# Performance work log

Hardware: AMD Instinct MI355X
Metric: run time of the kernel (lower is better)

The kernel has to match this reference:

```python
import jax, jax.numpy as jnp
import numpy as np


def setup_inputs() -> dict:
    key = jax.random.key(0)
    k1, k2 = jax.random.split(key)
    B, C, O, N = 16, 16, 16, 256
    in_tensor = jax.random.normal(k1, (B, C, N, N, 2), dtype=jnp.float32)
    # xavier_normal_ on (C, O, 15): fan_in = O*15, fan_out = C*15 (torch convention)
    std = (2.0 / (O * 15 + C * 15)) ** 0.5
    weights = jax.random.normal(k2, (C, O, 15), dtype=jnp.float32) * std
    return {"in_tensor": in_tensor, "weights": weights}


def reference(in_tensor, weights):
    # in_tensor: (B, C, N, N, 2); weights: (C, O, 15); default mode (real scalar per basis)
    B, C, N, _, _ = in_tensor.shape
    O = weights.shape[1]
    idx = jnp.arange(N)

    # diag: (B, C, N, 2); col/row sums: (B, C, N, 2)
    diag = jnp.swapaxes(jnp.diagonal(in_tensor, axis1=2, axis2=3), 2, 3)
    col_sum = in_tensor.sum(axis=2)
    row_sum = in_tensor.sum(axis=3)

    # class 3 maps: default mode uses only weight index 13 (index 14 unused, as in source)
    t = jnp.einsum('co,bcijk->boijk', weights[..., 13], in_tensor)
    out = t + jnp.swapaxes(t, 2, 3)

    def class1(out, v, A):
        # v: (B, C, 2), A: (C, O, 2)
        u0 = jnp.einsum('co,bck->bok', A[..., 0], v)  # broadcast everywhere
        u1 = jnp.einsum('co,bck->bok', A[..., 1], v)  # on diagonal
        out = out + u0[:, :, None, None, :]
        out = out.at[:, :, idx, idx, :].add(
            jnp.broadcast_to(u1[:, :, None, :], (B, O, N, 2)))
        return out

    def class2(out, v, A):
        # v: (B, C, N, 2), A: (C, O, 3)
        d = jnp.einsum('co,bcmk->bomk', A[..., 0], v)  # diagonal values
        r = jnp.einsum('co,bcmk->bomk', A[..., 1], v)  # broadcast over rows (index j)
        c = jnp.einsum('co,bcmk->bomk', A[..., 2], v)  # broadcast over cols (index i)
        out = out.at[:, :, idx, idx, :].add(d)
        out = out + r[:, :, None, :, :]
        out = out + c[:, :, :, None, :]
        return out

    out = class1(out, diag.mean(axis=2), weights[..., 0:2])
    out = class1(out, in_tensor.sum(axis=(2, 3)), weights[..., 0:2])
    out = class2(out, diag, weights[..., 4:7])
    out = class2(out, col_sum, weights[..., 7:10])
    out = class2(out, row_sum, weights[..., 10:13])
    return out
```

## Files before the change

kernel.cpp:

```cpp
#include <hip/hip_runtime.h>

#define NN 256
#define CC 16
#define OO 16
#define BB 16
#define NTILE 16
#define NPAIRS 136

#define OFF_DIAG 0
#define OFF_COL  131072
#define OFF_ROW  262144
#define OFF_TOT  393216
#define OFF_DSUM 393728
#define OFF_RI   394496
#define OFF_CJ   525568
#define OFF_DM   656640
#define OFF_S0   787712

__device__ __forceinline__ float2 nt_load2(const float2* p) {
    double d = __builtin_nontemporal_load((const double*)p);
    float2 r; *(double*)&r = d; return r;
}
__device__ __forceinline__ void nt_store2(float2* p, float2 v) {
    double d; *(float2*)&d = v;
    __builtin_nontemporal_store(d, (double*)p);
}

__global__ __launch_bounds__(1024) void k_reduce(const float* __restrict__ in,
                                                 float* __restrict__ ws) {
    float* diagA = ws + OFF_DIAG;
    float* colA  = ws + OFF_COL;
    float* rowA  = ws + OFF_ROW;
    float* totA  = ws + OFF_TOT;
    float* dsumA = ws + OFF_DSUM;

    const int bc  = blockIdx.x;
    const int tid = threadIdx.x;
    const int wv  = tid >> 6;
    const int ln  = tid & 63;

    const float* base = in + (size_t)bc * (NN * NN * 2);

    __shared__ float colLDS[16][512];
    __shared__ float rowLDS[512];
    __shared__ float diagLDS[512];
    __shared__ float redT[16][2];
    __shared__ float redD[16][2];

    float a0 = 0, a1 = 0, a2 = 0, a3 = 0;
    float b0 = 0, b1 = 0, b2 = 0, b3 = 0;
    float dsx = 0, dsy = 0;

    for (int i = wv; i < NN; i += 16) {
        const float4* rowp = (const float4*)(base + i * (NN * 2));
        float4 v0 = rowp[ln];
        float4 v1 = rowp[64 + ln];
        a0 += v0.x; a1 += v0.y; a2 += v0.z; a3 += v0.w;
        b0 += v1.x; b1 += v1.y; b2 += v1.z; b3 += v1.w;
        float sx = v0.x + v0.z + v1.x + v1.z;
        float sy = v0.y + v0.w + v1.y + v1.w;
#pragma unroll
        for (int off = 32; off >= 1; off >>= 1) {
            sx += __shfl_xor(sx, off);
            sy += __shfl_xor(sy, off);
        }
        if (ln == 0) { rowLDS[i * 2] = sx; rowLDS[i * 2 + 1] = sy; }
        int k4 = i >> 1;
        if (ln == (k4 & 63)) {
            float4 dv = (k4 >> 6) ? v1 : v0;
            float dx = (i & 1) ? dv.z : dv.x;
            float dy = (i & 1) ? dv.w : dv.y;
            diagLDS[i * 2] = dx; diagLDS[i * 2 + 1] = dy;
            dsx += dx; dsy += dy;
        }
    }
    colLDS[wv][4 * ln]       = a0; colLDS[wv][4 * ln + 1]       = a1;
    colLDS[wv][4 * ln + 2]   = a2; colLDS[wv][4 * ln + 3]       = a3;
    colLDS[wv][256 + 4 * ln]     = b0; colLDS[wv][256 + 4 * ln + 1] = b1;
    colLDS[wv][256 + 4 * ln + 2] = b2; colLDS[wv][256 + 4 * ln + 3] = b3;

#pragma unroll
    for (int off = 32; off >= 1; off >>= 1) {
        dsx += __shfl_xor(dsx, off);
        dsy += __shfl_xor(dsy, off);
    }
    if (ln == 0) { redD[wv][0] = dsx; redD[wv][1] = dsy; }
    __syncthreads();

    float totpart = 0.f;
    if (tid < 512) {
        float s = 0.f;
#pragma unroll
        for (int w2 = 0; w2 < 16; w2++) s += colLDS[w2][tid];
        colA[bc * 512 + tid]  = s;
        rowA[bc * 512 + tid]  = rowLDS[tid];
        diagA[bc * 512 + tid] = diagLDS[tid];
        totpart = s;
    }
#pragma unroll
    for (int off = 32; off >= 2; off >>= 1) totpart += __shfl_xor(totpart, off);
    if (ln < 2) redT[wv][ln] = totpart;
    __syncthreads();
    if (tid == 0) {
        float t0 = 0, t1 = 0, d0 = 0, d1 = 0;
        for (int w2 = 0; w2 < 16; w2++) {
            t0 += redT[w2][0]; t1 += redT[w2][1];
            d0 += redD[w2][0]; d1 += redD[w2][1];
        }
        totA[bc * 2]  = t0; totA[bc * 2 + 1]  = t1;
        dsumA[bc * 2] = d0; dsumA[bc * 2 + 1] = d1;
    }
}

__global__ __launch_bounds__(256) void k_terms(const float* __restrict__ w,
                                               float* __restrict__ ws) {
    const float* diagA = ws + OFF_DIAG;
    const float* colA  = ws + OFF_COL;
    const float* rowA  = ws + OFF_ROW;
    const float* totA  = ws + OFF_TOT;
    const float* dsumA = ws + OFF_DSUM;
    float* RiA = ws + OFF_RI;
    float* CjA = ws + OFF_CJ;
    float* DmA = ws + OFF_DM;
    float* S0A = ws + OFF_S0;

    const int b = blockIdx.x >> 4;
    const int o = blockIdx.x & 15;
    const int m = threadIdx.x;

    __shared__ float wL[CC][15];
    if (m < CC * 15) wL[m / 15][m % 15] = w[(m / 15) * (OO * 15) + o * 15 + m % 15];
    __syncthreads();

    float rix = 0, riy = 0, cjx = 0, cjy = 0, dmx = 0, dmy = 0;
    float s0x = 0, s0y = 0, dcx = 0, dcy = 0;
#pragma unroll
    for (int c = 0; c < CC; c++) {
        int bcm = (b * CC + c) * NN + m;
        float2 dg = ((const float2*)diagA)[bcm];
        float2 cs = ((const float2*)colA)[bcm];
        float2 rs = ((const float2*)rowA)[bcm];
        float w4 = wL[c][4], w5 = wL[c][5], w6 = wL[c][6];
        float w7 = wL[c][7], w8 = wL[c][8], w9 = wL[c][9];
        float wa = wL[c][10], wb = wL[c][11], wc = wL[c][12];
        rix += w6 * dg.x + w9 * cs.x + wc * rs.x;
        riy += w6 * dg.y + w9 * cs.y + wc * rs.y;
        cjx += w5 * dg.x + w8 * cs.x + wb * rs.x;
        cjy += w5 * dg.y + w8 * cs.y + wb * rs.y;
        dmx += w4 * dg.x + w7 * cs.x + wa * rs.x;
        dmy += w4 * dg.y + w7 * cs.y + wa * rs.y;
        float2 tt = ((const float2*)totA)[b * CC + c];
        float2 dd = ((const float2*)dsumA)[b * CC + c];
        float vx = dd.x * (1.0f / NN) + tt.x;
        float vy = dd.y * (1.0f / NN) + tt.y;
        s0x += wL[c][0] * vx; s0y += wL[c][0] * vy;
        dcx += wL[c][1] * vx; dcy += wL[c][1] * vy;
    }
    int om = (b * OO + o) * NN + m;
    ((float2*)RiA)[om] = make_float2(rix, riy);
    ((float2*)CjA)[om] = make_float2(cjx, cjy);
    ((float2*)DmA)[om] = make_float2(dmx + dcx, dmy + dcy);
    if (m == 0) ((float2*)S0A)[b * OO + o] = make_float2(s0x, s0y);
}

__global__ __launch_bounds__(256) void k_main(const float* __restrict__ in,
                                              const float* __restrict__ w,
                                              float* __restrict__ out,
                                              const float* __restrict__ ws) {
    const float* RiA  = ws + OFF_RI;
    const float* CjA  = ws + OFF_CJ;
    const float* DmA  = ws + OFF_DM;
    const float* S0A  = ws + OFF_S0;

    const int b = blockIdx.x / NPAIRS;
    int p = blockIdx.x % NPAIRS;
    int I = 0;
    { int cnt = NTILE; while (p >= cnt) { p -= cnt; cnt--; I++; } }
    const int J = I + p;

    const int tid = threadIdx.x;
    const int ti = tid >> 4;
    const int tj = tid & 15;

    __shared__ float  xch[256 * 34];
    __shared__ float  wsm[256];
    __shared__ float2 s0L[16];
    __shared__ float2 RiI[16][16];
    __shared__ float2 CjJ[16][16];
    __shared__ float2 RiJ[16][16];
    __shared__ float2 CjI[16][16];

    {
        wsm[tid] = w[tid * 15 + 13];
        RiI[ti][tj] = ((const float2*)RiA)[(b * OO + ti) * NN + I * 16 + tj];
        CjJ[ti][tj] = ((const float2*)CjA)[(b * OO + ti) * NN + J * 16 + tj];
        if (I != J) {
            RiJ[ti][tj] = ((const float2*)RiA)[(b * OO + ti) * NN + J * 16 + tj];
            CjI[ti][tj] = ((const float2*)CjA)[(b * OO + ti) * NN + I * 16 + tj];
        }
        if (tid < 16) s0L[tid] = ((const float2*)S0A)[b * OO + tid];
    }
    __syncthreads();

    float2 P[16], Q[16];
#pragma unroll
    for (int o = 0; o < 16; o++) { P[o] = make_float2(0.f, 0.f); Q[o] = make_float2(0.f, 0.f); }

    const float2* pA = (const float2*)in + ((b * CC) * NN + I * 16 + ti) * NN + J * 16 + tj;
    const float2* pB = (const float2*)in + ((b * CC) * NN + J * 16 + ti) * NN + I * 16 + tj;

#pragma unroll 8
    for (int c = 0; c < CC; c++) {
        float2 a  = nt_load2(&pA[c * (NN * NN)]);
        float2 bb = nt_load2(&pB[c * (NN * NN)]);
#pragma unroll
        for (int o = 0; o < 16; o++) {
            float wv = wsm[c * 16 + o];
            P[o].x += wv * a.x;  P[o].y += wv * a.y;
            Q[o].x += wv * bb.x; Q[o].y += wv * bb.y;
        }
    }

    const int sidx = ti * 16 + (tj ^ ti);
    const int ridx = tj * 16 + (ti ^ tj);
    const bool dgl = (I == J) && (ti == tj);

#pragma unroll
    for (int o = 0; o < 16; o++) *(float2*)&xch[sidx * 34 + o * 2] = Q[o];
    __syncthreads();
    {
        const int gi = I * 16 + ti, gj = J * 16 + tj;
#pragma unroll
        for (int o = 0; o < 16; o++) {
            float2 qt = *(const float2*)&xch[ridx * 34 + o * 2];
            float2 s0 = s0L[o];
            float2 ri = RiI[o][ti];
            float2 cj = CjJ[o][tj];
            float vx = P[o].x + qt.x + s0.x + ri.x + cj.x;
            float vy = P[o].y + qt.y + s0.y + ri.y + cj.y;
            if (dgl) {
                float2 dm = ((const float2*)DmA)[(b * OO + o) * NN + gi];
                vx += dm.x; vy += dm.y;
            }
            nt_store2(((float2*)out) + ((b * OO + o) * NN + gi) * NN + gj,
                      make_float2(vx, vy));
        }
    }

    if (I == J) return;

    __syncthreads();

#pragma unroll
    for (int o = 0; o < 16; o++) *(float2*)&xch[sidx * 34 + o * 2] = P[o];
    __syncthreads();
    {
        const int gi = J * 16 + ti, gj = I * 16 + tj;
#pragma unroll
        for (int o = 0; o < 16; o++) {
            float2 pt = *(const float2*)&xch[ridx * 34 + o * 2];
            float2 s0 = s0L[o];
            float2 ri = RiJ[o][ti];
            float2 cj = CjI[o][tj];
            float vx = Q[o].x + pt.x + s0.x + ri.x + cj.x;
            float vy = Q[o].y + pt.y + s0.y + ri.y + cj.y;
            nt_store2(((float2*)out) + ((b * OO + o) * NN + gi) * NN + gj,
                      make_float2(vx, vy));
        }
    }
}

extern "C" void kernel_launch(void* const* d_in, const int* in_sizes, int n_in,
                              void* d_out, int out_size, void* d_ws, size_t ws_size,
                              hipStream_t stream) {
    const float* in = (const float*)d_in[0];
    const float* w  = (const float*)d_in[1];
    float* out = (float*)d_out;
    float* ws  = (float*)d_ws;

    hipLaunchKernelGGL(k_reduce, dim3(BB * CC), dim3(1024), 0, stream, in, ws);
    hipLaunchKernelGGL(k_terms,  dim3(BB * OO), dim3(256),  0, stream, w, ws);
    hipLaunchKernelGGL(k_main,   dim3(BB * NPAIRS), dim3(256), 0, stream, in, w, out, ws);
}
```

Measured before the change: 266.3 us.

## Split reduce blocks in half, shrink main-kernel LDS exchange, fold S0 into Ri

The reduction kernel now splits each (b,c) plane into two half-plane blocks, which doubles the grid to 512 blocks for better CU coverage. Partial column sums and totals are written to separate buffers and combined in k_terms. The main kernel folds the S0 scalar into the Ri term. It also exchanges the transposed tile in two 8-channel chunks through a half-size LDS buffer, uses packed float2 vector arithmetic, and sets launch bounds for 4 blocks per CU to raise occupancy. The cost is extra barriers in the epilogue and extra partial-sum reads in k_terms.

```diff
diff --git a/kernel.cpp b/kernel.cpp
--- a/kernel.cpp
+++ b/kernel.cpp
@@ -7,43 +7,53 @@
 #define NTILE 16
 #define NPAIRS 136
 
-#define OFF_DIAG 0
-#define OFF_COL  131072
-#define OFF_ROW  262144
-#define OFF_TOT  393216
-#define OFF_DSUM 393728
-#define OFF_RI   394496
-#define OFF_CJ   525568
-#define OFF_DM   656640
-#define OFF_S0   787712
-
-__device__ __forceinline__ float2 nt_load2(const float2* p) {
+#define OFF_DIAG  0
+#define OFF_ROW   131072
+#define OFF_COL0  262144
+#define OFF_COL1  393216
+#define OFF_TOT0  524288
+#define OFF_TOT1  524800
+#define OFF_DSUM0 525312
+#define OFF_DSUM1 525824
+#define OFF_RI    526336
+#define OFF_CJ    657408
+#define OFF_DM    788480
+
+typedef float v2f __attribute__((ext_vector_type(2)));
+
+__device__ __forceinline__ v2f nt_loadv(const float2* p) {
     double d = __builtin_nontemporal_load((const double*)p);
-    float2 r; *(double*)&r = d; return r;
-}
-__device__ __forceinline__ void nt_store2(float2* p, float2 v) {
-    double d; *(float2*)&d = v;
+    v2f r; __builtin_memcpy(&r, &d, 8); return r;
+}
+__device__ __forceinline__ void nt_storev(float2* p, v2f v) {
+    double d; __builtin_memcpy(&d, &v, 8);
     __builtin_nontemporal_store(d, (double*)p);
+}
+__device__ __forceinline__ v2f ld2(const float* p) {
+    v2f r; __builtin_memcpy(&r, p, 8); return r;
 }
 
 __global__ __launch_bounds__(1024) void k_reduce(const float* __restrict__ in,
                                                  float* __restrict__ ws) {
     float* diagA = ws + OFF_DIAG;
-    float* colA  = ws + OFF_COL;
     float* rowA  = ws + OFF_ROW;
-    float* totA  = ws + OFF_TOT;
-    float* dsumA = ws + OFF_DSUM;
-
-    const int bc  = blockIdx.x;
+
+    const int bid  = blockIdx.x;
+    const int bc   = bid >> 1;
+    const int half = bid & 1;
+    float* colH  = ws + (half ? OFF_COL1 : OFF_COL0);
+    float* totH  = ws + (half ? OFF_TOT1 : OFF_TOT0);
+    float* dsumH = ws + (half ? OFF_DSUM1 : OFF_DSUM0);
+
     const int tid = threadIdx.x;
     const int wv  = tid >> 6;
     const int ln  = tid & 63;
 
-    const float* base = in + (size_t)bc * (NN * NN * 2);
+    const float* base = in + (size_t)bc * (NN * NN * 2) + (size_t)half * (128 * NN * 2);
 
     __shared__ float colLDS[16][512];
-    __shared__ float rowLDS[512];
-    __shared__ float diagLDS[512];
+    __shared__ float rowLDS[256];
+    __shared__ float diagLDS[256];
     __shared__ float redT[16][2];
     __shared__ float redD[16][2];
 
@@ -51,7 +61,10 @@
     float b0 = 0, b1 = 0, b2 = 0, b3 = 0;
     float dsx = 0, dsy = 0;
 
-    for (int i = wv; i < NN; i += 16) {
+#pragma unroll 2
+    for (int k = 0; k < 8; k++) {
+        const int i = wv + 16 * k;
+        const int g = (half << 7) + i;
         const float4* rowp = (const float4*)(base + i * (NN * 2));
         float4 v0 = rowp[ln];
         float4 v1 = rowp[64 + ln];
@@ -64,20 +77,18 @@
             sx += __shfl_xor(sx, off);
             sy += __shfl_xor(sy, off);
         }
-        if (ln == 0) { rowLDS[i * 2] = sx; rowLDS[i * 2 + 1] = sy; }
-        int k4 = i >> 1;
+        if (ln == 0) { rowLDS[2 * i] = sx; rowLDS[2 * i + 1] = sy; }
+        const int k4 = g >> 1;
         if (ln == (k4 & 63)) {
-            float4 dv = (k4 >> 6) ? v1 : v0;
-            float dx = (i & 1) ? dv.z : dv.x;
-            float dy = (i & 1) ? dv.w : dv.y;
-            diagLDS[i * 2] = dx; diagLDS[i * 2 + 1] = dy;
+            float4 dv = (k4 & 64) ? v1 : v0;
+            float dx = (g & 1) ? dv.z : dv.x;
+            float dy = (g & 1) ? dv.w : dv.y;
+            diagLDS[2 * i] = dx; diagLDS[2 * i + 1] = dy;
             dsx += dx; dsy += dy;
         }
     }
-    colLDS[wv][4 * ln]       = a0; colLDS[wv][4 * ln + 1]       = a1;
-    colLDS[wv][4 * ln + 2]   = a2; colLDS[wv][4 * ln + 3]       = a3;
-    colLDS[wv][256 + 4 * ln]     = b0; colLDS[wv][256 + 4 * ln + 1] = b1;
-    colLDS[wv][256 + 4 * ln + 2] = b2; colLDS[wv][256 + 4 * ln + 3] = b3;
+    ((float4*)&colLDS[wv][0])[ln]   = make_float4(a0, a1, a2, a3);
+    ((float4*)&colLDS[wv][256])[ln] = make_float4(b0, b1, b2, b3);
 
 #pragma unroll
     for (int off = 32; off >= 1; off >>= 1) {
@@ -92,10 +103,12 @@
         float s = 0.f;
 #pragma unroll
         for (int w2 = 0; w2 < 16; w2++) s += colLDS[w2][tid];
-        colA[bc * 512 + tid]  = s;
-        rowA[bc * 512 + tid]  = rowLDS[tid];
-        diagA[bc * 512 + tid] = diagLDS[tid];
+        colH[bc * 512 + tid] = s;
         totpart = s;
+    }
+    if (tid < 256) {
+        rowA[bc * 512 + half * 256 + tid]  = rowLDS[tid];
+        diagA[bc * 512 + half * 256 + tid] = diagLDS[tid];
     }
 #pragma unroll
     for (int off = 32; off >= 2; off >>= 1) totpart += __shfl_xor(totpart, off);
@@ -107,22 +120,24 @@
             t0 += redT[w2][0]; t1 += redT[w2][1];
             d0 += redD[w2][0]; d1 += redD[w2][1];
         }
-        totA[bc * 2]  = t0; totA[bc * 2 + 1]  = t1;
-        dsumA[bc * 2] = d0; dsumA[bc * 2 + 1] = d1;
+        totH[bc * 2]  = t0; totH[bc * 2 + 1]  = t1;
+        dsumH[bc * 2] = d0; dsumH[bc * 2 + 1] = d1;
     }
 }
 
 __global__ __launch_bounds__(256) void k_terms(const float* __restrict__ w,
                                                float* __restrict__ ws) {
     const float* diagA = ws + OFF_DIAG;
-    const float* colA  = ws + OFF_COL;
     const float* rowA  = ws + OFF_ROW;
-    const float* totA  = ws + OFF_TOT;
-    const float* dsumA = ws + OFF_DSUM;
+    const float* colA0 = ws + OFF_COL0;
+    const float* colA1 = ws + OFF_COL1;
+    const float* tot0  = ws + OFF_TOT0;
+    const float* tot1  = ws + OFF_TOT1;
+    const float* dsm0  = ws + OFF_DSUM0;
+    const float* dsm1  = ws + OFF_DSUM1;
     float* RiA = ws + OFF_RI;
     float* CjA = ws + OFF_CJ;
     float* DmA = ws + OFF_DM;
-    float* S0A = ws + OFF_S0;
 
     const int b = blockIdx.x >> 4;
     const int o = blockIdx.x & 15;
@@ -138,39 +153,41 @@
     for (int c = 0; c < CC; c++) {
         int bcm = (b * CC + c) * NN + m;
         float2 dg = ((const float2*)diagA)[bcm];
-        float2 cs = ((const float2*)colA)[bcm];
+        float2 c0 = ((const float2*)colA0)[bcm];
+        float2 c1 = ((const float2*)colA1)[bcm];
         float2 rs = ((const float2*)rowA)[bcm];
+        float csx = c0.x + c1.x, csy = c0.y + c1.y;
         float w4 = wL[c][4], w5 = wL[c][5], w6 = wL[c][6];
         float w7 = wL[c][7], w8 = wL[c][8], w9 = wL[c][9];
         float wa = wL[c][10], wb = wL[c][11], wc = wL[c][12];
-        rix += w6 * dg.x + w9 * cs.x + wc * rs.x;
-        riy += w6 * dg.y + w9 * cs.y + wc * rs.y;
-        cjx += w5 * dg.x + w8 * cs.x + wb * rs.x;
-        cjy += w5 * dg.y + w8 * cs.y + wb * rs.y;
-        dmx += w4 * dg.x + w7 * cs.x + wa * rs.x;
-        dmy += w4 * dg.y + w7 * cs.y + wa * rs.y;
-        float2 tt = ((const float2*)totA)[b * CC + c];
-        float2 dd = ((const float2*)dsumA)[b * CC + c];
-        float vx = dd.x * (1.0f / NN) + tt.x;
-        float vy = dd.y * (1.0f / NN) + tt.y;
+        rix += w6 * dg.x + w9 * csx + wc * rs.x;
+        riy += w6 * dg.y + w9 * csy + wc * rs.y;
+        cjx += w5 * dg.x + w8 * csx + wb * rs.x;
+        cjy += w5 * dg.y + w8 * csy + wb * rs.y;
+        dmx += w4 * dg.x + w7 * csx + wa * rs.x;
+        dmy += w4 * dg.y + w7 * csy + wa * rs.y;
+        float2 ta = ((const float2*)tot0)[b * CC + c];
+        float2 tb = ((const float2*)tot1)[b * CC + c];
+        float2 da = ((const float2*)dsm0)[b * CC + c];
+        float2 db = ((const float2*)dsm1)[b * CC + c];
+        float vx = (da.x + db.x) * (1.0f / NN) + ta.x + tb.x;
+        float vy = (da.y + db.y) * (1.0f / NN) + ta.y + tb.y;
         s0x += wL[c][0] * vx; s0y += wL[c][0] * vy;
         dcx += wL[c][1] * vx; dcy += wL[c][1] * vy;
     }
     int om = (b * OO + o) * NN + m;
-    ((float2*)RiA)[om] = make_float2(rix, riy);
+    ((float2*)RiA)[om] = make_float2(rix + s0x, riy + s0y);
     ((float2*)CjA)[om] = make_float2(cjx, cjy);
     ((float2*)DmA)[om] = make_float2(dmx + dcx, dmy + dcy);
-    if (m == 0) ((float2*)S0A)[b * OO + o] = make_float2(s0x, s0y);
-}
-
-__global__ __launch_bounds__(256) void k_main(const float* __restrict__ in,
-                                              const float* __restrict__ w,
-                                              float* __restrict__ out,
-                                              const float* __restrict__ ws) {
-    const float* RiA  = ws + OFF_RI;
-    const float* CjA  = ws + OFF_CJ;
-    const float* DmA  = ws + OFF_DM;
-    const float* S0A  = ws + OFF_S0;
+}
+
+__global__ __launch_bounds__(256, 4) void k_main(const float* __restrict__ in,
+                                                 const float* __restrict__ w,
+                                                 float* __restrict__ out,
+                                                 const float* __restrict__ ws) {
+    const float* RiA = ws + OFF_RI;
+    const float* CjA = ws + OFF_CJ;
+    const float* DmA = ws + OFF_DM;
 
     const int b = blockIdx.x / NPAIRS;
     int p = blockIdx.x % NPAIRS;
@@ -182,90 +199,82 @@
     const int ti = tid >> 4;
     const int tj = tid & 15;
 
-    __shared__ float  xch[256 * 34];
-    __shared__ float  wsm[256];
-    __shared__ float2 s0L[16];
-    __shared__ float2 RiI[16][16];
-    __shared__ float2 CjJ[16][16];
-    __shared__ float2 RiJ[16][16];
-    __shared__ float2 CjI[16][16];
+    __shared__ __align__(16) float xch[256 * 18];
+    __shared__ float wsm[256];
+    __shared__ v2f RiI[16][16];
+    __shared__ v2f CjJ[16][16];
+    __shared__ v2f RiJ[16][16];
+    __shared__ v2f CjI[16][16];
 
     {
         wsm[tid] = w[tid * 15 + 13];
-        RiI[ti][tj] = ((const float2*)RiA)[(b * OO + ti) * NN + I * 16 + tj];
-        CjJ[ti][tj] = ((const float2*)CjA)[(b * OO + ti) * NN + J * 16 + tj];
+        RiI[ti][tj] = ld2(RiA + 2 * ((b * OO + ti) * NN + I * 16 + tj));
+        CjJ[ti][tj] = ld2(CjA + 2 * ((b * OO + ti) * NN + J * 16 + tj));
         if (I != J) {
-            RiJ[ti][tj] = ((const float2*)RiA)[(b * OO + ti) * NN + J * 16 + tj];
-            CjI[ti][tj] = ((const float2*)CjA)[(b * OO + ti) * NN + I * 16 + tj];
-        }
-        if (tid < 16) s0L[tid] = ((const float2*)S0A)[b * OO + tid];
-    }
-    __syncthreads();
-
-    float2 P[16], Q[16];
-#pragma unroll
-    for (int o = 0; o < 16; o++) { P[o] = make_float2(0.f, 0.f); Q[o] = make_float2(0.f, 0.f); }
-
-    const float2* pA = (const float2*)in + ((b * CC) * NN + I * 16 + ti) * NN + J * 16 + tj;
-    const float2* pB = (const float2*)in + ((b * CC) * NN + J * 16 + ti) * NN + I * 16 + tj;
-
-#pragma unroll 8
+            RiJ[ti][tj] = ld2(RiA + 2 * ((b * OO + ti) * NN + J * 16 + tj));
+            CjI[ti][tj] = ld2(CjA + 2 * ((b * OO + ti) * NN + I * 16 + tj));
+        }
+    }
+    __syncthreads();
+
+    v2f P[16], Q[16];
+#pragma unroll
+    for (int o = 0; o < 16; o++) { P[o] = (v2f)(0.f); Q[o] = (v2f)(0.f); }
+
+    const float2* pA = (const float2*)in + ((size_t)(b * CC) * NN + I * 16 + ti) * NN + J * 16 + tj;
+    const float2* pB = (const float2*)in + ((size_t)(b * CC) * NN + J * 16 + ti) * NN + I * 16 + tj;
+
+#pragma unroll 4
     for (int c = 0; c < CC; c++) {
-        float2 a  = nt_load2(&pA[c * (NN * NN)]);
-        float2 bb = nt_load2(&pB[c * (NN * NN)]);
+        v2f a  = nt_loadv(&pA[(size_t)c * (NN * NN)]);
+        v2f bb = nt_loadv(&pB[(size_t)c * (NN * NN)]);
 #pragma unroll
         for (int o = 0; o < 16; o++) {
             float wv = wsm[c * 16 + o];
-            P[o].x += wv * a.x;  P[o].y += wv * a.y;
-            Q[o].x += wv * bb.x; Q[o].y += wv * bb.y;
+            P[o] += wv * a;
+            Q[o] += wv * bb;
         }
     }
 
     const int sidx = ti * 16 + (tj ^ ti);
     const int ridx = tj * 16 + (ti ^ tj);
     const bool dgl = (I == J) && (ti == tj);
-
-#pragma unroll
-    for (int o = 0; o < 16; o++) *(float2*)&xch[sidx * 34 + o * 2] = Q[o];
-    __syncthreads();
+    float2* out2 = (float2*)out;
+
     {
         const int gi = I * 16 + ti, gj = J * 16 + tj;
-#pragma unroll
-        for (int o = 0; o < 16; o++) {
-            float2 qt = *(const float2*)&xch[ridx * 34 + o * 2];
-            float2 s0 = s0L[o];
-            float2 ri = RiI[o][ti];
-            float2 cj = CjJ[o][tj];
-            float vx = P[o].x + qt.x + s0.x + ri.x + cj.x;
-            float vy = P[o].y + qt.y + s0.y + ri.y + cj.y;
-            if (dgl) {
-                float2 dm = ((const float2*)DmA)[(b * OO + o) * NN + gi];
-                vx += dm.x; vy += dm.y;
+        for (int oc = 0; oc < 16; oc += 8) {
+#pragma unroll
+            for (int k = 0; k < 8; k++) *(v2f*)&xch[sidx * 18 + 2 * k] = Q[oc + k];
+            __syncthreads();
+#pragma unroll
+            for (int k = 0; k < 8; k++) {
+                const int o = oc + k;
+                v2f qt = *(const v2f*)&xch[ridx * 18 + 2 * k];
+                v2f v = P[o] + qt + RiI[o][ti] + CjJ[o][tj];
+                if (dgl) v += ld2(DmA + 2 * ((b * OO + o) * NN + gi));
+                nt_storev(&out2[((size_t)(b * OO + o) * NN + gi) * NN + gj], v);
             }
-            nt_store2(((float2*)out) + ((b * OO + o) * NN + gi) * NN + gj,
-                      make_float2(vx, vy));
+            __syncthreads();
         }
     }
 
     if (I == J) return;
 
-    __syncthreads();
-
-#pragma unroll
-    for (int o = 0; o < 16; o++) *(float2*)&xch[sidx * 34 + o * 2] = P[o];
-    __syncthreads();
     {
         const int gi = J * 16 + ti, gj = I * 16 + tj;
-#pragma unroll
-        for (int o = 0; o < 16; o++) {
-            float2 pt = *(const float2*)&xch[ridx * 34 + o * 2];
-            float2 s0 = s0L[o];
-            float2 ri = RiJ[o][ti];
-            float2 cj = CjI[o][tj];
-            float vx = Q[o].x + pt.x + s0.x + ri.x + cj.x;
-            float vy = Q[o].y + pt.y + s0.y + ri.y + cj.y;
-            nt_store2(((float2*)out) + ((b * OO + o) * NN + gi) * NN + gj,
-                      make_float2(vx, vy));
+        for (int oc = 0; oc < 16; oc += 8) {
+#pragma unroll
+            for (int k = 0; k < 8; k++) *(v2f*)&xch[sidx * 18 + 2 * k] = P[oc + k];
+            __syncthreads();
+#pragma unroll
+            for (int k = 0; k < 8; k++) {
+                const int o = oc + k;
+                v2f pt = *(const v2f*)&xch[ridx * 18 + 2 * k];
+                v2f v = Q[o] + pt + RiJ[o][ti] + CjI[o][tj];
+                nt_storev(&out2[((size_t)(b * OO + o) * NN + gi) * NN + gj], v);
+            }
+            if (oc == 0) __syncthreads();
         }
     }
 }
@@ -278,7 +287,7 @@
     float* out = (float*)d_out;
     float* ws  = (float*)d_ws;
 
-    hipLaunchKernelGGL(k_reduce, dim3(BB * CC), dim3(1024), 0, stream, in, ws);
-    hipLaunchKernelGGL(k_terms,  dim3(BB * OO), dim3(256),  0, stream, w, ws);
-    hipLaunchKernelGGL(k_main,   dim3(BB * NPAIRS), dim3(256), 0, stream, in, w, out, ws);
-}
+    hipLaunchKernelGGL(k_reduce, dim3(BB * CC * 2), dim3(1024), 0, stream, in, ws);
+    hipLaunchKernelGGL(k_terms,  dim3(BB * OO),     dim3(256),  0, stream, w, ws);
+    hipLaunchKernelGGL(k_main,   dim3(BB * NPAIRS), dim3(256),  0, stream, in, w, out, ws);
+}
```

Result: no change. 268.0 us (+0.7%).
